# Optimization experiments

Measured on AMD Instinct MI355X. Metric: run time of the kernel, lower is better.

Reference implementation:

```python
import jax, jax.numpy as jnp
import numpy as np

B, S, D = 2, 2048, 4096
H, KVH = 32, 8
DH = D // H  # 128
N_REP = H // KVH
ROPE_BASE = 10000.0


def _rope_tables(seq_len, d_head, dtype):
    inv_freq = 1.0 / (ROPE_BASE ** (jnp.arange(0, d_head, 2, dtype=jnp.float32) / d_head))
    pos = jnp.arange(seq_len, dtype=jnp.float32)
    freqs = pos[:, None] * inv_freq[None, :]            # (S, DH/2)
    emb = jnp.concatenate([freqs, freqs], axis=-1)       # (S, DH)
    return jnp.cos(emb).astype(dtype), jnp.sin(emb).astype(dtype)


def _rotate_half(x):
    half = x.shape[-1] // 2
    return jnp.concatenate([-x[..., half:], x[..., :half]], axis=-1)


def _apply_rope(x, cos, sin):
    # x: (B, h, S, DH); cos/sin: (S, DH)
    return x * cos[None, None, :, :] + _rotate_half(x) * sin[None, None, :, :]


def setup_inputs() -> dict:
    key = jax.random.key(0)
    ks = jax.random.split(key, 6)
    scale = 0.02
    return {
        "x": jax.random.normal(ks[0], (B, S, D), dtype=jnp.float32),
        "Wq": jax.random.normal(ks[1], (D, H * DH), dtype=jnp.float32) * scale,
        "Wk": jax.random.normal(ks[2], (D, KVH * DH), dtype=jnp.float32) * scale,
        "Wv": jax.random.normal(ks[3], (D, KVH * DH), dtype=jnp.float32) * scale,
        "Wo": jax.random.normal(ks[4], (D, D), dtype=jnp.float32) * scale,
        "bo": jnp.zeros((D,), dtype=jnp.float32),
    }


def reference(x, Wq, Wk, Wv, Wo, bo):
    b, s, _ = x.shape
    # QKV projections (no bias)
    q = (x @ Wq).reshape(b, s, H, DH).transpose(0, 2, 1, 3)    # (B, H, S, DH)
    k = (x @ Wk).reshape(b, s, KVH, DH).transpose(0, 2, 1, 3)  # (B, KVH, S, DH)
    v = (x @ Wv).reshape(b, s, KVH, DH).transpose(0, 2, 1, 3)
    # RoPE on q and k
    cos, sin = _rope_tables(s, DH, x.dtype)
    q = _apply_rope(q, cos, sin)
    k = _apply_rope(k, cos, sin)
    # GQA: repeat KV heads to match query heads
    k = jnp.repeat(k, N_REP, axis=1)  # (B, H, S, DH)
    v = jnp.repeat(v, N_REP, axis=1)
    # Causal scaled dot-product attention
    scale = 1.0 / jnp.sqrt(jnp.asarray(DH, dtype=x.dtype))
    scores = jnp.einsum("bhqd,bhkd->bhqk", q, k) * scale       # (B, H, S, S)
    causal = jnp.tril(jnp.ones((s, s), dtype=bool))
    scores = jnp.where(causal[None, None, :, :], scores, jnp.finfo(x.dtype).min)
    attn = jax.nn.softmax(scores, axis=-1)
    out = jnp.einsum("bhqk,bhkd->bhqd", attn, v)               # (B, H, S, DH)
    out = out.transpose(0, 2, 1, 3).reshape(b, s, H * DH)
    return out @ Wo + bo
```

## Files before the change

kernel.cpp:

```cpp
#include <hip/hip_runtime.h>

typedef unsigned short u16;
typedef unsigned int u32;
typedef __attribute__((ext_vector_type(8))) short s16x8;
typedef __attribute__((ext_vector_type(8))) u16 u16x8;
typedef __attribute__((ext_vector_type(4))) float f32x4;
typedef __attribute__((ext_vector_type(4))) u32 u32x4;

#define SEQ 2048
#define NH 32
#define NKV 8

__device__ __forceinline__ u16 f2bf(float f) {
  union { float f; u32 u; } v; v.f = f;
  u32 r = v.u + 0x7FFFu + ((v.u >> 16) & 1u);
  return (u16)(r >> 16);
}
__device__ __forceinline__ float bf2f(u16 u) {
  union { u32 u; float f; } v; v.u = ((u32)u) << 16;
  return v.f;
}
__device__ __forceinline__ u32 pack2(float a, float b) {
  return (u32)f2bf(a) | ((u32)f2bf(b) << 16);
}
__device__ __forceinline__ void gll16(u16* lds, const u16* g) {
  __builtin_amdgcn_global_load_lds(
      (const __attribute__((address_space(1))) u32*)g,
      (__attribute__((address_space(3))) u32*)lds, 16, 0, 0);
}

__global__ void k_conv_bf16(const float* __restrict__ in, u16* __restrict__ out) {
  long i = ((long)blockIdx.x * 256 + threadIdx.x) * 4;
  const float4 v = *(const float4*)&in[i];
  ushort4 ov = { f2bf(v.x), f2bf(v.y), f2bf(v.z), f2bf(v.w) };
  *(ushort4*)&out[i] = ov;
}

__global__ void k_transpose_bf16(const float* __restrict__ W, u16* __restrict__ Wt,
                                 int K, int N) {
  __shared__ u16 T[64 * 65];
  int n0 = blockIdx.x * 64, k0 = blockIdx.y * 64;
  int t = threadIdx.x;
  int cr = t >> 4, cc = (t & 15) * 4;
#pragma unroll
  for (int r2 = 0; r2 < 4; ++r2) {
    int k = cr + r2 * 16;
    const float4 v = *(const float4*)&W[(long)(k0 + k) * N + n0 + cc];
    u16* d = &T[k * 65 + cc];
    d[0] = f2bf(v.x); d[1] = f2bf(v.y); d[2] = f2bf(v.z); d[3] = f2bf(v.w);
  }
  __syncthreads();
#pragma unroll
  for (int r2 = 0; r2 < 4; ++r2) {
    int n = cr + r2 * 16;
    ushort4 ov = { T[(cc + 0) * 65 + n], T[(cc + 1) * 65 + n],
                   T[(cc + 2) * 65 + n], T[(cc + 3) * 65 + n] };
    *(ushort4*)&Wt[(long)(n0 + n) * K + k0 + cc] = ov;
  }
}

__global__ void k_vt(const u16* __restrict__ Vb, u16* __restrict__ Vt) {
  __shared__ u16 T[64][136];
  int s0 = blockIdx.x * 64;
  int g = blockIdx.y;
  const u16* src = Vb + (long)g * SEQ * 128;
  u16* dst = Vt + (long)g * 128 * SEQ;
  int t = threadIdx.x;
#pragma unroll
  for (int i = 0; i < 4; ++i) {
    int c = i * 256 + t;
    int row = c >> 4, col8 = (c & 15) * 8;
    u16x8 v = *(const u16x8*)&src[(long)(s0 + row) * 128 + col8];
#pragma unroll
    for (int j = 0; j < 8; ++j) T[row][col8 + j] = v[j];
  }
  __syncthreads();
#pragma unroll
  for (int i = 0; i < 4; ++i) {
    int c = i * 256 + t;
    int d = c >> 3, k8 = (c & 7) * 8;
    u16x8 v;
#pragma unroll
    for (int j = 0; j < 8; ++j) v[j] = T[k8 + j][d];
    *(u16x8*)&dst[(long)d * SEQ + s0 + k8] = v;
  }
}

__global__ void k_rope_table(float* __restrict__ cosT, float* __restrict__ sinT) {
  int id = blockIdx.x * 256 + threadIdx.x;
  int s = id >> 6, i = id & 63;
  float inv = powf(10000.0f, -(float)i * (1.0f / 64.0f));
  float f = (float)s * inv;
  float sv, cv;
  sincosf(f, &sv, &cv);
  cosT[id] = cv; sinT[id] = sv;
}

__global__ void k_rope_apply(u16* __restrict__ Qb, u16* __restrict__ Kb,
                             const float* __restrict__ cosT, const float* __restrict__ sinT) {
  int id = blockIdx.x * 256 + threadIdx.x;
  int i = id & 63;
  int row = id >> 6;
  u16* base = (row < 131072) ? (Qb + (long)row * 128) : (Kb + (long)(row - 131072) * 128);
  int s = row & (SEQ - 1);
  float c = cosT[s * 64 + i], sn = sinT[s * 64 + i];
  float x0 = bf2f(base[i]), x1 = bf2f(base[i + 64]);
  base[i] = f2bf(x0 * c - x1 * sn);
  base[i + 64] = f2bf(x1 * c + x0 * sn);
}

template <int MODE>
__global__ __launch_bounds__(256, 2) void k_gemm_bt(
    const u16* __restrict__ A, const u16* __restrict__ Bt,
    float* __restrict__ Cf, const float* __restrict__ bias,
    u16* __restrict__ Qb, u16* __restrict__ Kb, u16* __restrict__ Vb,
    int K, int nbn) {
  __shared__ u16 As[128 * 32];
  __shared__ u16 Bs[128 * 32];
  int bid = blockIdx.x;
  int cpx = (int)gridDim.x >> 3;
  int swz = (bid & 7) * cpx + (bid >> 3);
  int bm = swz / nbn, bn = swz - bm * nbn;
  int tid = threadIdx.x;
  int lane = tid & 63, wave = tid >> 6;
  int lo = lane & 15, hi = lane >> 4;
  int wm = (wave >> 1) * 64, wn = (wave & 1) * 64;
  f32x4 zero4 = {0.f, 0.f, 0.f, 0.f};
  f32x4 acc[4][4];
#pragma unroll
  for (int m = 0; m < 4; ++m)
#pragma unroll
    for (int n = 0; n < 4; ++n) acc[m][n] = zero4;
  const u16* Ab = A + (long)bm * 128 * K;
  const u16* Bb = Bt + (long)bn * 128 * K;
  for (int kt = 0; kt < K; kt += 32) {
#pragma unroll
    for (int j = 0; j < 2; ++j) {
      int e = (j * 256 + tid) * 8;
      int row = e >> 5, col = e & 31;
      gll16(&As[e], &Ab[(long)row * K + kt + col]);
      gll16(&Bs[e], &Bb[(long)row * K + kt + col]);
    }
    __syncthreads();
    s16x8 af[4], bf[4];
#pragma unroll
    for (int m = 0; m < 4; ++m) af[m] = *(const s16x8*)&As[(wm + m * 16 + lo) * 32 + hi * 8];
#pragma unroll
    for (int n = 0; n < 4; ++n) bf[n] = *(const s16x8*)&Bs[(wn + n * 16 + lo) * 32 + hi * 8];
#pragma unroll
    for (int m = 0; m < 4; ++m)
#pragma unroll
      for (int n = 0; n < 4; ++n)
        acc[m][n] = __builtin_amdgcn_mfma_f32_16x16x32_bf16(af[m], bf[n], acc[m][n], 0, 0, 0);
    __syncthreads();
  }
#pragma unroll
  for (int m = 0; m < 4; ++m) {
#pragma unroll
    for (int n = 0; n < 4; ++n) {
      int colg = bn * 128 + wn + n * 16 + lo;
#pragma unroll
      for (int r = 0; r < 4; ++r) {
        int rowg = bm * 128 + wm + m * 16 + hi * 4 + r;
        float v = acc[m][n][r];
        if (MODE == 1) {
          Cf[(long)rowg * 4096 + colg] = v + bias[colg];
        } else {
          int bb = rowg >> 11, s = rowg & 2047;
          u16 u = f2bf(v);
          int d = colg & 127;
          if (colg < 4096) {
            int hh = colg >> 7;
            Qb[(((long)bb * NH + hh) * SEQ + s) * 128 + d] = u;
          } else if (colg < 5120) {
            int hh = (colg - 4096) >> 7;
            Kb[(((long)bb * NKV + hh) * SEQ + s) * 128 + d] = u;
          } else {
            int hh = (colg - 5120) >> 7;
            Vb[(((long)bb * NKV + hh) * SEQ + s) * 128 + d] = u;
          }
        }
      }
    }
  }
}

__device__ __forceinline__ void stage_load(u32x4* kr_, u32x4* vr_,
    const u16* __restrict__ Kg, const u16* __restrict__ Vg, int kt, int tid) {
#pragma unroll
  for (int i = 0; i < 4; ++i) {
    int idx = i * 256 + tid;
    int kr = idx >> 4, kc = idx & 15;
    kr_[i] = *(const u32x4*)&Kg[(long)(kt + kr) * 128 + kc * 8];
    int vr = idx >> 3, vc = idx & 7;
    vr_[i] = *(const u32x4*)&Vg[(long)vr * SEQ + kt + vc * 8];
  }
}
__device__ __forceinline__ void stage_write(const u32x4* kr_, const u32x4* vr_,
    u16* Ks, u16* Vs, int tid) {
  char* KsB = (char*)Ks; char* VsB = (char*)Vs;
#pragma unroll
  for (int i = 0; i < 4; ++i) {
    int idx = i * 256 + tid;
    int kr = idx >> 4, kc = idx & 15;
    *(u32x4*)(KsB + ((kr * 256 + kc * 16) ^ ((kr & 7) << 4))) = kr_[i];
    int vr = idx >> 3, vc = idx & 7;
    *(u32x4*)(VsB + ((vr * 128 + vc * 16) ^ ((vr & 7) << 4))) = vr_[i];
  }
}

__global__ __launch_bounds__(256, 2) void k_attn(
    const u16* __restrict__ Qb, const u16* __restrict__ Kb,
    const u16* __restrict__ Vt, u16* __restrict__ AO) {
  __shared__ u16 Ks0[64 * 128], Ks1[64 * 128], Vs0[128 * 64], Vs1[128 * 64];
  __shared__ u16 Ps[4][2][16][32];
  int gid = blockIdx.x;
  int wid = (gid & 7) * 128 + (gid >> 3);
  int g = wid >> 6, w = wid & 63;
  int b = g >> 3, kvh = g & 7;
  int h = kvh * 4 + (w >> 4);
  int qt = 15 - (w & 15);
  int qb0 = qt * 128;
  int tid = threadIdx.x, lane = tid & 63, wave = tid >> 6;
  int lo = lane & 15, hi = lane >> 4;
  int q0w = qb0 + wave * 32;

  const u16* Kg = Kb + (long)(b * NKV + kvh) * SEQ * 128;
  const u16* Vg = Vt + (long)(b * NKV + kvh) * 128 * SEQ;
  const u16* Qg = Qb + (long)(b * NH + h) * SEQ * 128;

  s16x8 qf[2][4];
#pragma unroll
  for (int qs = 0; qs < 2; ++qs)
#pragma unroll
    for (int ds = 0; ds < 4; ++ds)
      qf[qs][ds] = *(const s16x8*)&Qg[(long)(q0w + qs * 16 + lo) * 128 + ds * 32 + hi * 8];

  f32x4 zero4 = {0.f, 0.f, 0.f, 0.f};
  f32x4 o[2][8];
#pragma unroll
  for (int qs = 0; qs < 2; ++qs)
#pragma unroll
    for (int dt = 0; dt < 8; ++dt) o[qs][dt] = zero4;
  float m_run[2] = {-1e30f, -1e30f};
  float l_run[2] = {0.f, 0.f};
  const float scale = 0.088388347648318447f;

  char* PsQ0 = (char*)&Ps[wave][0][0][0];
  char* PsQ1 = (char*)&Ps[wave][1][0][0];
  int pbase = lo << 6;

  u32x4 kreg[4], vreg[4];
  int ntiles = (qb0 >> 6) + 2;
  stage_load(kreg, vreg, Kg, Vg, 0, tid);
  stage_write(kreg, vreg, Ks0, Vs0, tid);
  __syncthreads();

  for (int t = 0; t < ntiles; ++t) {
    int kt = t << 6;
    u16* Ks = (t & 1) ? Ks1 : Ks0;
    u16* Vs = (t & 1) ? Vs1 : Vs0;
    bool more = (t + 1 < ntiles);
    if (more) stage_load(kreg, vreg, Kg, Vg, (t + 1) << 6, tid);
    if (kt <= q0w + 31) {
      f32x4 sa[2][4];
#pragma unroll
      for (int qs = 0; qs < 2; ++qs)
#pragma unroll
        for (int a = 0; a < 4; ++a) sa[qs][a] = zero4;
#pragma unroll
      for (int ds = 0; ds < 4; ++ds) {
        s16x8 kf[4];
#pragma unroll
        for (int a = 0; a < 4; ++a)
          kf[a] = *(const s16x8*)&Ks[((a * 16 + lo) << 7) + (((ds * 4 + hi) ^ (lo & 7)) << 3)];
#pragma unroll
        for (int qs = 0; qs < 2; ++qs)
#pragma unroll
          for (int a = 0; a < 4; ++a)
            sa[qs][a] = __builtin_amdgcn_mfma_f32_16x16x32_bf16(kf[a], qf[qs][ds], sa[qs][a], 0, 0, 0);
      }
      bool pmask = (kt + 63) > q0w;
      u32 pp[2][4][2];
#pragma unroll
      for (int qs = 0; qs < 2; ++qs) {
        float pv[16];
        int qrow = q0w + qs * 16 + lo;
#pragma unroll
        for (int a = 0; a < 4; ++a)
#pragma unroll
          for (int r = 0; r < 4; ++r) {
            float s = sa[qs][a][r] * scale;
            if (pmask && (kt + a * 16 + hi * 4 + r) > qrow) s = -1e30f;
            pv[a * 4 + r] = s;
          }
        float mx = pv[0];
#pragma unroll
        for (int i = 1; i < 16; ++i) mx = fmaxf(mx, pv[i]);
        mx = fmaxf(mx, __shfl_xor(mx, 16));
        mx = fmaxf(mx, __shfl_xor(mx, 32));
        float mnew = fmaxf(m_run[qs], mx);
        if (!__all(mnew - m_run[qs] <= 8.0f)) {
          float corr = __expf(m_run[qs] - mnew);
          m_run[qs] = mnew;
          l_run[qs] *= corr;
#pragma unroll
          for (int dt = 0; dt < 8; ++dt)
#pragma unroll
            for (int r = 0; r < 4; ++r) o[qs][dt][r] *= corr;
        }
        float sum = 0.f;
#pragma unroll
        for (int i = 0; i < 16; ++i) { pv[i] = __expf(pv[i] - m_run[qs]); sum += pv[i]; }
        sum += __shfl_xor(sum, 16);
        sum += __shfl_xor(sum, 32);
        l_run[qs] += sum;
#pragma unroll
        for (int a = 0; a < 4; ++a) {
          pp[qs][a][0] = pack2(pv[a * 4 + 0], pv[a * 4 + 1]);
          pp[qs][a][1] = pack2(pv[a * 4 + 2], pv[a * 4 + 3]);
        }
      }
#pragma unroll
      for (int kb = 0; kb < 2; ++kb) {
#pragma unroll
        for (int qs = 0; qs < 2; ++qs) {
          char* Pw = qs ? PsQ1 : PsQ0;
#pragma unroll
          for (int al = 0; al < 2; ++al) {
            uint2 wv; wv.x = pp[qs][kb * 2 + al][0]; wv.y = pp[qs][kb * 2 + al][1];
            *(uint2*)(Pw + pbase + (((al * 4 + hi) ^ (lo & 7)) << 3)) = wv;
          }
        }
        asm volatile("s_waitcnt lgkmcnt(0)" ::: "memory");
        __builtin_amdgcn_sched_barrier(0);
        union { uint2 u2[2]; s16x8 v; } bu0, bu1;
        bu0.u2[0] = *(uint2*)(PsQ0 + pbase + (((hi * 2 + 0) ^ (lo & 7)) << 3));
        bu0.u2[1] = *(uint2*)(PsQ0 + pbase + (((hi * 2 + 1) ^ (lo & 7)) << 3));
        bu1.u2[0] = *(uint2*)(PsQ1 + pbase + (((hi * 2 + 0) ^ (lo & 7)) << 3));
        bu1.u2[1] = *(uint2*)(PsQ1 + pbase + (((hi * 2 + 1) ^ (lo & 7)) << 3));
#pragma unroll
        for (int dt = 0; dt < 8; ++dt) {
          s16x8 vf = *(const s16x8*)((char*)Vs +
              (((dt * 16 + lo) * 128 + (kb * 4 + hi) * 16) ^ ((lo & 7) << 4)));
          o[0][dt] = __builtin_amdgcn_mfma_f32_16x16x32_bf16(vf, bu0.v, o[0][dt], 0, 0, 0);
          o[1][dt] = __builtin_amdgcn_mfma_f32_16x16x32_bf16(vf, bu1.v, o[1][dt], 0, 0, 0);
        }
      }
    }
    if (more) stage_write(kreg, vreg, (t & 1) ? Ks0 : Ks1, (t & 1) ? Vs0 : Vs1, tid);
    __syncthreads();
  }

#pragma unroll
  for (int qs = 0; qs < 2; ++qs) {
    float inv = 1.0f / l_run[qs];
    long base = ((long)(b * SEQ + q0w + qs * 16 + lo)) * 4096 + h * 128;
#pragma unroll
    for (int dt = 0; dt < 8; ++dt) {
      uint2 wv;
      wv.x = pack2(o[qs][dt][0] * inv, o[qs][dt][1] * inv);
      wv.y = pack2(o[qs][dt][2] * inv, o[qs][dt][3] * inv);
      *(uint2*)&AO[base + dt * 16 + hi * 4] = wv;
    }
  }
}

extern "C" void kernel_launch(void* const* d_in, const int* in_sizes, int n_in,
                              void* d_out, int out_size, void* d_ws, size_t ws_size,
                              hipStream_t stream) {
  const float* x  = (const float*)d_in[0];
  const float* Wq = (const float*)d_in[1];
  const float* Wk = (const float*)d_in[2];
  const float* Wv = (const float*)d_in[3];
  const float* Wo = (const float*)d_in[4];
  const float* bo = (const float*)d_in[5];
  float* out = (float*)d_out;

  char* ws = (char*)d_ws;
  u16* xb     = (u16*)(ws);
  u16* Wt     = (u16*)(ws + 33554432);
  u16* Vtb    = (u16*)(ws + 67108864);
  u16* Qb     = (u16*)(ws + 83886080);
  u16* Kb     = (u16*)(ws + 117440512);
  u16* Vb     = (u16*)(ws + 125829120);
  float* cosT = (float*)(ws + 134217728);
  float* sinT = (float*)(ws + 134742016);
  if (ws_size < 135266304) return;
  u16* AO  = xb;
  u16* Wto = Wt;

  k_conv_bf16<<<16384, 256, 0, stream>>>(x, xb);
  k_transpose_bf16<<<dim3(64, 64), 256, 0, stream>>>(Wq, Wt, 4096, 4096);
  k_transpose_bf16<<<dim3(16, 64), 256, 0, stream>>>(Wk, Wt + (long)4096 * 4096, 4096, 1024);
  k_transpose_bf16<<<dim3(16, 64), 256, 0, stream>>>(Wv, Wt + (long)5120 * 4096, 4096, 1024);
  k_rope_table<<<512, 256, 0, stream>>>(cosT, sinT);
  k_gemm_bt<0><<<1536, 256, 0, stream>>>(xb, Wt, nullptr, nullptr, Qb, Kb, Vb, 4096, 48);
  k_vt<<<dim3(32, 16), 256, 0, stream>>>(Vb, Vtb);
  k_rope_apply<<<40960, 256, 0, stream>>>(Qb, Kb, cosT, sinT);
  k_transpose_bf16<<<dim3(64, 64), 256, 0, stream>>>(Wo, Wto, 4096, 4096);
  k_attn<<<1024, 256, 0, stream>>>(Qb, Kb, Vtb, AO);
  k_gemm_bt<1><<<1024, 256, 0, stream>>>(AO, Wto, out, bo, nullptr, nullptr, nullptr, 4096, 32);
}
```

Baseline: 684.7 us.

## Replace 128x128 GEMM with 256x256 tile, 512-thread, multi-stage LDS pipelined kernel

Replaces the simple single-buffered 128x128 GEMM with a 256x256 tile kernel using 512 threads, 128KB dynamic LDS double-buffered across 64-wide K steps. Global-to-LDS loads for upcoming K-slices are issued between MFMA phases, and an XOR swizzle is applied to LDS layout to avoid bank conflicts. The aim is to hide memory latency and raise arithmetic intensity for the QKV and output projections. In exchange occupancy drops to one block per CU, the grid gets smaller (384/256 blocks), and the hand-written waitcnt logic is fragile.

```diff
diff --git a/kernel.cpp b/kernel.cpp
--- a/kernel.cpp
+++ b/kernel.cpp
@@ -109,14 +109,49 @@
   base[i + 64] = f2bf(x1 * c + x0 * sn);
 }
 
+__device__ __forceinline__ void stg(char* smem, int base, const u16* XG, long off,
+                                    int K, int tid, int r0, int scol) {
+  gll16((u16*)(smem + base + tid * 16), XG + (long)r0 * K + off + scol);
+  gll16((u16*)(smem + base + 8192 + tid * 16), XG + (long)(r0 + 128) * K + off + scol);
+}
+
+#define GPHASE(MH, KH, READB, STG_STMT, WAIT_STMT)                                  \
+  {                                                                                 \
+    const char* Ab_ = smem + cbuf + (KH) * 16384;                                   \
+    const char* Bb_ = smem + cbuf + 32768 + (KH) * 16384;                           \
+    s16x8 Ar_[4];                                                                   \
+    _Pragma("unroll")                                                               \
+    for (int m_ = 0; m_ < 4; ++m_)                                                  \
+      Ar_[m_] = *(const s16x8*)(Ab_ + aoff + ((MH) * 4 + m_) * 1024);               \
+    if (READB) {                                                                    \
+      _Pragma("unroll")                                                             \
+      for (int n_ = 0; n_ < 4; ++n_)                                                \
+        Br[n_] = *(const s16x8*)(Bb_ + boff + n_ * 1024);                           \
+    }                                                                               \
+    STG_STMT;                                                                       \
+    __builtin_amdgcn_s_barrier();                                                   \
+    asm volatile("s_waitcnt lgkmcnt(0)" ::: "memory");                              \
+    __builtin_amdgcn_sched_barrier(0);                                              \
+    __builtin_amdgcn_s_setprio(1);                                                  \
+    _Pragma("unroll")                                                               \
+    for (int m_ = 0; m_ < 4; ++m_) {                                                \
+      _Pragma("unroll")                                                             \
+      for (int n_ = 0; n_ < 4; ++n_)                                                \
+        acc[(MH) * 4 + m_][n_] = __builtin_amdgcn_mfma_f32_16x16x32_bf16(           \
+            Ar_[m_], Br[n_], acc[(MH) * 4 + m_][n_], 0, 0, 0);                      \
+    }                                                                               \
+    __builtin_amdgcn_s_setprio(0);                                                  \
+    WAIT_STMT;                                                                      \
+    __builtin_amdgcn_s_barrier();                                                   \
+  }
+
 template <int MODE>
-__global__ __launch_bounds__(256, 2) void k_gemm_bt(
+__global__ __launch_bounds__(512, 1) void k_gemm256(
     const u16* __restrict__ A, const u16* __restrict__ Bt,
     float* __restrict__ Cf, const float* __restrict__ bias,
     u16* __restrict__ Qb, u16* __restrict__ Kb, u16* __restrict__ Vb,
     int K, int nbn) {
-  __shared__ u16 As[128 * 32];
-  __shared__ u16 Bs[128 * 32];
+  extern __shared__ char smem[];
   int bid = blockIdx.x;
   int cpx = (int)gridDim.x >> 3;
   int swz = (bid & 7) * cpx + (bid >> 3);
@@ -124,45 +159,61 @@
   int tid = threadIdx.x;
   int lane = tid & 63, wave = tid >> 6;
   int lo = lane & 15, hi = lane >> 4;
-  int wm = (wave >> 1) * 64, wn = (wave & 1) * 64;
+  int wm = wave >> 2, wn = wave & 3;
+  const u16* Ag = A + (long)bm * 256 * K;
+  const u16* Bg = Bt + (long)bn * 256 * K;
   f32x4 zero4 = {0.f, 0.f, 0.f, 0.f};
-  f32x4 acc[4][4];
-#pragma unroll
-  for (int m = 0; m < 4; ++m)
+  f32x4 acc[8][4];
+#pragma unroll
+  for (int m = 0; m < 8; ++m)
 #pragma unroll
     for (int n = 0; n < 4; ++n) acc[m][n] = zero4;
-  const u16* Ab = A + (long)bm * 128 * K;
-  const u16* Bb = Bt + (long)bn * 128 * K;
-  for (int kt = 0; kt < K; kt += 32) {
-#pragma unroll
-    for (int j = 0; j < 2; ++j) {
-      int e = (j * 256 + tid) * 8;
-      int row = e >> 5, col = e & 31;
-      gll16(&As[e], &Ab[(long)row * K + kt + col]);
-      gll16(&Bs[e], &Bb[(long)row * K + kt + col]);
-    }
-    __syncthreads();
-    s16x8 af[4], bf[4];
-#pragma unroll
-    for (int m = 0; m < 4; ++m) af[m] = *(const s16x8*)&As[(wm + m * 16 + lo) * 32 + hi * 8];
-#pragma unroll
-    for (int n = 0; n < 4; ++n) bf[n] = *(const s16x8*)&Bs[(wn + n * 16 + lo) * 32 + hi * 8];
-#pragma unroll
-    for (int m = 0; m < 4; ++m)
-#pragma unroll
-      for (int n = 0; n < 4; ++n)
-        acc[m][n] = __builtin_amdgcn_mfma_f32_16x16x32_bf16(af[m], bf[n], acc[m][n], 0, 0, 0);
-    __syncthreads();
-  }
-#pragma unroll
-  for (int m = 0; m < 4; ++m) {
+
+  int aoff = (wm * 128 + lo) * 64 + ((hi ^ (lo & 3)) << 4);
+  int boff = (wn * 64 + lo) * 64 + ((hi ^ (lo & 3)) << 4);
+  int r0 = tid >> 2;
+  int scol = (((tid & 3) ^ (r0 & 3)) << 3);
+
+  int nt = K >> 6;
+  stg(smem, 0,             Ag, 0,  K, tid, r0, scol);
+  stg(smem, 32768,         Bg, 0,  K, tid, r0, scol);
+  stg(smem, 16384,         Ag, 32, K, tid, r0, scol);
+  stg(smem, 49152,         Bg, 32, K, tid, r0, scol);
+  stg(smem, 65536,         Ag, 64, K, tid, r0, scol);
+  stg(smem, 65536 + 32768, Bg, 64, K, tid, r0, scol);
+  asm volatile("s_waitcnt vmcnt(4)" ::: "memory");
+  __builtin_amdgcn_s_barrier();
+
+  s16x8 Br[4];
+  for (int t = 0; t < nt; ++t) {
+    int cbuf = (t & 1) << 16;
+    int obuf = cbuf ^ 65536;
+    long k1 = (long)(t + 1) * 64;
+    long k2 = (long)(t + 2) * 64;
+    bool s1ok = (t + 1) < nt, s2ok = (t + 2) < nt;
+    GPHASE(0, 0, true,
+           { if (s1ok) stg(smem, obuf + 16384, Ag, k1 + 32, K, tid, r0, scol); }, {})
+    GPHASE(1, 0, false,
+           { if (s1ok) stg(smem, obuf + 49152, Bg, k1 + 32, K, tid, r0, scol); }, {})
+    GPHASE(0, 1, true,
+           { if (s2ok) stg(smem, cbuf, Ag, k2, K, tid, r0, scol); }, {})
+    GPHASE(1, 1, false,
+           { if (s2ok) stg(smem, cbuf + 32768, Bg, k2, K, tid, r0, scol); },
+           {
+             if (s2ok)      asm volatile("s_waitcnt vmcnt(4)" ::: "memory");
+             else if (s1ok) asm volatile("s_waitcnt vmcnt(0)" ::: "memory");
+           })
+  }
+
+#pragma unroll
+  for (int mr = 0; mr < 8; ++mr) {
 #pragma unroll
     for (int n = 0; n < 4; ++n) {
-      int colg = bn * 128 + wn + n * 16 + lo;
+      int colg = bn * 256 + wn * 64 + n * 16 + lo;
 #pragma unroll
       for (int r = 0; r < 4; ++r) {
-        int rowg = bm * 128 + wm + m * 16 + hi * 4 + r;
-        float v = acc[m][n][r];
+        int rowg = bm * 256 + wm * 128 + mr * 16 + hi * 4 + r;
+        float v = acc[mr][n][r];
         if (MODE == 1) {
           Cf[(long)rowg * 4096 + colg] = v + bias[colg];
         } else {
@@ -390,15 +441,20 @@
   u16* AO  = xb;
   u16* Wto = Wt;
 
+  (void)hipFuncSetAttribute((const void*)k_gemm256<0>,
+                            hipFuncAttributeMaxDynamicSharedMemorySize, 131072);
+  (void)hipFuncSetAttribute((const void*)k_gemm256<1>,
+                            hipFuncAttributeMaxDynamicSharedMemorySize, 131072);
+
   k_conv_bf16<<<16384, 256, 0, stream>>>(x, xb);
   k_transpose_bf16<<<dim3(64, 64), 256, 0, stream>>>(Wq, Wt, 4096, 4096);
   k_transpose_bf16<<<dim3(16, 64), 256, 0, stream>>>(Wk, Wt + (long)4096 * 4096, 4096, 1024);
   k_transpose_bf16<<<dim3(16, 64), 256, 0, stream>>>(Wv, Wt + (long)5120 * 4096, 4096, 1024);
   k_rope_table<<<512, 256, 0, stream>>>(cosT, sinT);
-  k_gemm_bt<0><<<1536, 256, 0, stream>>>(xb, Wt, nullptr, nullptr, Qb, Kb, Vb, 4096, 48);
+  k_gemm256<0><<<384, 512, 131072, stream>>>(xb, Wt, nullptr, nullptr, Qb, Kb, Vb, 4096, 24);
   k_vt<<<dim3(32, 16), 256, 0, stream>>>(Vb, Vtb);
   k_rope_apply<<<40960, 256, 0, stream>>>(Qb, Kb, cosT, sinT);
   k_transpose_bf16<<<dim3(64, 64), 256, 0, stream>>>(Wo, Wto, 4096, 4096);
   k_attn<<<1024, 256, 0, stream>>>(Qb, Kb, Vtb, AO);
-  k_gemm_bt<1><<<1024, 256, 0, stream>>>(AO, Wto, out, bo, nullptr, nullptr, nullptr, 4096, 32);
-}
+  k_gemm256<1><<<256, 512, 131072, stream>>>(AO, Wto, out, bo, nullptr, nullptr, nullptr, 4096, 16);
+}
```

Result: faster. 639.7 us (-6.6%).
